# Performance work log

Hardware: AMD Instinct MI355X
Metric: run time of the kernel (lower is better)

## Reference

```python
import jax, jax.numpy as jnp
import numpy as np

# Llama-3-8B-like attention layer with ragged KV-cache attention (tp_size=1).
B = 4          # number of sequences in the ragged batch
NEW = 512      # new tokens per sequence
CACHE = 4096   # existing KV-cache length per sequence
TOTAL = CACHE + NEW
H = 32         # query heads
HKV = 8        # kv heads (GQA)
G = H // HKV   # query heads per kv head
D = 128        # head dim
HID = 4096     # hidden size
BSZ = B * NEW  # total ragged tokens
EPS = 1e-6
ROPE_THETA = 10000.0


def rotate_half(x):
    x1, x2 = jnp.split(x, 2, axis=-1)
    return jnp.concatenate([-x2, x1], axis=-1)


def setup_inputs() -> dict:
    key = jax.random.key(0)
    ks = jax.random.split(key, 8)
    hidden_states = jax.random.normal(ks[0], (BSZ, HID), jnp.float32)
    # per-token absolute positions: each sequence continues from CACHE
    pos = jnp.tile(CACHE + jnp.arange(NEW), B).astype(jnp.float32)  # [BSZ]
    inv_freq = 1.0 / (ROPE_THETA ** (jnp.arange(0, D, 2, dtype=jnp.float32) / D))
    ang = pos[:, None] * inv_freq[None, :]              # [BSZ, D/2]
    emb = jnp.concatenate([ang, ang], axis=-1)          # [BSZ, D]
    cos, sin = jnp.cos(emb), jnp.sin(emb)
    ln_weight = jnp.ones((HID,), jnp.float32)
    wq = jax.random.normal(ks[1], (HID, H * D), jnp.float32) * 0.02
    wk = jax.random.normal(ks[2], (HID, HKV * D), jnp.float32) * 0.02
    wv = jax.random.normal(ks[3], (HID, HKV * D), jnp.float32) * 0.02
    wo = jax.random.normal(ks[4], (H * D, HID), jnp.float32) * 0.02
    # pre-populated KV cache (first CACHE slots are live history; tail gets overwritten)
    k_cache = jax.random.normal(ks[5], (B, TOTAL, HKV, D), jnp.float32) * 0.5
    v_cache = jax.random.normal(ks[6], (B, TOTAL, HKV, D), jnp.float32) * 0.5
    return {"hidden_states": hidden_states, "cos": cos, "sin": sin,
            "ln_weight": ln_weight, "wq": wq, "wk": wk, "wv": wv, "wo": wo,
            "k_cache": k_cache, "v_cache": v_cache}


def reference(hidden_states, cos, sin, ln_weight, wq, wk, wv, wo, k_cache, v_cache):
    residual = hidden_states
    # RMSNorm (fp32 math, as in the torch module)
    x = hidden_states.astype(jnp.float32)
    var = jnp.mean(x * x, axis=-1, keepdims=True)
    hn = ln_weight * (x * jax.lax.rsqrt(var + EPS))
    # QKV projections (ragged: [tokens, heads, D])
    q = (hn @ wq).reshape(BSZ, H, D)
    k = (hn @ wk).reshape(BSZ, HKV, D)
    v = (hn @ wv).reshape(BSZ, HKV, D)
    # RoPE with unsqueeze_dim=1
    c, s = cos[:, None, :], sin[:, None, :]
    q = q * c + rotate_half(q) * s
    k = k * c + rotate_half(k) * s
    # un-ragged view: [B, NEW, heads, D]
    qb = q.reshape(B, NEW, H, D)
    kb = k.reshape(B, NEW, HKV, D)
    vb = v.reshape(B, NEW, HKV, D)
    # append new K/V into the cache
    kc = k_cache.at[:, CACHE:TOTAL].set(kb)
    vc = v_cache.at[:, CACHE:TOTAL].set(vb)
    # GQA attention against full cache, causal over absolute positions
    qg = qb.reshape(B, NEW, HKV, G, D)
    scores = jnp.einsum('bqhgd,bshd->bhgqs', qg, kc) * (1.0 / np.sqrt(D))
    qpos = CACHE + jnp.arange(NEW)
    mask = jnp.arange(TOTAL)[None, :] <= qpos[:, None]       # [NEW, TOTAL]
    scores = jnp.where(mask[None, None, None], scores, -1e30)
    p = jax.nn.softmax(scores, axis=-1)
    out = jnp.einsum('bhgqs,bshd->bqhgd', p, vc).reshape(BSZ, H * D)
    o = out @ wo
    return residual + o
```

## Files before the change

### kernel.cpp

```cpp
#include <hip/hip_runtime.h>
#include <hip/hip_bf16.h>

typedef __attribute__((ext_vector_type(8))) short short8;
typedef __attribute__((ext_vector_type(4))) float floatx4;
typedef __attribute__((ext_vector_type(16))) float f32x16;

#define B_C 4
#define NEW_C 512
#define CACHE_C 4096
#define TOTAL_C 4608
#define H_C 32
#define HKV_C 8
#define D_C 128
#define HID_C 4096
#define QKV_N 6144

__device__ __forceinline__ unsigned short f2bf(float f) {
  union { float f; unsigned u; } v; v.f = f;
  unsigned r = v.u + 0x7FFFu + ((v.u >> 16) & 1u);
  return (unsigned short)(r >> 16);
}
__device__ __forceinline__ float bf2f(unsigned short h) {
  union { unsigned u; float f; } v; v.u = ((unsigned)h) << 16; return v.f;
}
__device__ __forceinline__ unsigned pack_bf16(float lo, float hi) {
  return ((unsigned)f2bf(hi) << 16) | (unsigned)f2bf(lo);
}
__device__ __forceinline__ unsigned pack_trunc(float lo, float hi) {
  union { float f; unsigned u; } a, b;
  a.f = lo; b.f = hi;
  return __builtin_amdgcn_perm(b.u, a.u, 0x07060302u);
}
__device__ __forceinline__ void gload_lds16(const unsigned short* g, unsigned short* lds) {
  __builtin_amdgcn_global_load_lds(
      (const __attribute__((address_space(1))) unsigned int*)g,
      (__attribute__((address_space(3))) unsigned int*)lds, 16, 0, 0);
}

__global__ __launch_bounds__(256) void rmsnorm_k(const float* __restrict__ x,
                                                 const float* __restrict__ g,
                                                 unsigned short* __restrict__ hn) {
  const int row = blockIdx.x;
  const int t = threadIdx.x;
  const float4* xr = (const float4*)(x + (size_t)row * 4096);
  float4 v[4];
  float ss = 0.f;
#pragma unroll
  for (int i = 0; i < 4; ++i) {
    v[i] = xr[t + i * 256];
    ss += v[i].x * v[i].x + v[i].y * v[i].y + v[i].z * v[i].z + v[i].w * v[i].w;
  }
#pragma unroll
  for (int m = 1; m < 64; m <<= 1) ss += __shfl_xor(ss, m);
  __shared__ float red[4];
  if ((t & 63) == 0) red[t >> 6] = ss;
  __syncthreads();
  ss = red[0] + red[1] + red[2] + red[3];
  const float inv = rsqrtf(ss * (1.f / 4096.f) + 1e-6f);
  const float4* gw = (const float4*)g;
#pragma unroll
  for (int i = 0; i < 4; ++i) {
    float4 w4 = gw[t + i * 256];
    ushort4 o;
    o.x = f2bf(v[i].x * inv * w4.x);
    o.y = f2bf(v[i].y * inv * w4.y);
    o.z = f2bf(v[i].z * inv * w4.z);
    o.w = f2bf(v[i].w * inv * w4.w);
    *(ushort4*)&hn[(size_t)row * 4096 + (t + i * 256) * 4] = o;
  }
}

__global__ __launch_bounds__(256) void build_wqkvT_k(const float* __restrict__ wq,
                                                     const float* __restrict__ wk,
                                                     const float* __restrict__ wv,
                                                     unsigned short* __restrict__ out) {
  __shared__ float tile[32][33];
  const int n0 = blockIdx.x * 32, k0 = blockIdx.y * 32;
  const float* src; int ld, nc;
  if (n0 < 4096)      { src = wq; ld = 4096; nc = n0; }
  else if (n0 < 5120) { src = wk; ld = 1024; nc = n0 - 4096; }
  else                { src = wv; ld = 1024; nc = n0 - 5120; }
  const int t = threadIdx.x, r = t >> 3, cv = (t & 7) * 4;
  const float4 v = *(const float4*)&src[(size_t)(k0 + r) * ld + nc + cv];
  tile[r][cv + 0] = v.x; tile[r][cv + 1] = v.y; tile[r][cv + 2] = v.z; tile[r][cv + 3] = v.w;
  __syncthreads();
  ushort4 o;
  o.x = f2bf(tile[cv + 0][r]); o.y = f2bf(tile[cv + 1][r]);
  o.z = f2bf(tile[cv + 2][r]); o.w = f2bf(tile[cv + 3][r]);
  *(ushort4*)&out[(size_t)(n0 + r) * 4096 + k0 + cv] = o;
}

__global__ __launch_bounds__(256) void transpose_cvt_k(const float* __restrict__ src,
                                                       long sbs_hi, long sbs_lo, int sld,
                                                       unsigned short* __restrict__ dst,
                                                       long dbs, int dld) {
  __shared__ float tile[32][33];
  const int z = blockIdx.z;
  const long sb = (long)(z >> 3) * sbs_hi + (long)(z & 7) * sbs_lo;
  const long db = (long)z * dbs;
  const int r0 = blockIdx.y * 32, c0 = blockIdx.x * 32;
  const int t = threadIdx.x, r = t >> 3, cv = (t & 7) * 4;
  const float4 v = *(const float4*)&src[sb + (long)(r0 + r) * sld + c0 + cv];
  tile[r][cv + 0] = v.x; tile[r][cv + 1] = v.y; tile[r][cv + 2] = v.z; tile[r][cv + 3] = v.w;
  __syncthreads();
  ushort4 o;
  o.x = f2bf(tile[cv + 0][r]); o.y = f2bf(tile[cv + 1][r]);
  o.z = f2bf(tile[cv + 2][r]); o.w = f2bf(tile[cv + 3][r]);
  *(ushort4*)&dst[db + (long)(c0 + r) * dld + r0 + cv] = o;
}

__global__ __launch_bounds__(256) void transpose_u16_k(const unsigned short* __restrict__ src,
                                                       long sbs, int sld,
                                                       unsigned short* __restrict__ dst,
                                                       long dbs, int dld) {
  __shared__ unsigned short tile[32][36];
  const int z = blockIdx.z;
  const long sb = (long)z * sbs;
  const long db = (long)z * dbs;
  const int r0 = blockIdx.y * 32, c0 = blockIdx.x * 32;
  const int t = threadIdx.x, r = t >> 3, cv = (t & 7) * 4;
  const ushort4 v = *(const ushort4*)&src[sb + (long)(r0 + r) * sld + c0 + cv];
  tile[r][cv + 0] = v.x; tile[r][cv + 1] = v.y; tile[r][cv + 2] = v.z; tile[r][cv + 3] = v.w;
  __syncthreads();
  ushort4 o;
  o.x = tile[cv + 0][r]; o.y = tile[cv + 1][r]; o.z = tile[cv + 2][r]; o.w = tile[cv + 3][r];
  *(ushort4*)&dst[db + (long)(c0 + r) * dld + r0 + cv] = o;
}

__global__ __launch_bounds__(256) void cvt_kcache_k(const float* __restrict__ kc,
                                                    unsigned short* __restrict__ Kall) {
  const long i = (long)blockIdx.x * 256 + threadIdx.x;
  const long c = i & 31, s = (i >> 5) & 4095, h = (i >> 17) & 7, b = i >> 20;
  const float4 v = *(const float4*)&kc[((b * 4608 + s) * 8 + h) * 128 + c * 4];
  ushort4 o;
  o.x = f2bf(v.x); o.y = f2bf(v.y); o.z = f2bf(v.z); o.w = f2bf(v.w);
  *(ushort4*)&Kall[((b * 8 + h) * 4608L + s) * 128 + c * 4] = o;
}

__global__ __launch_bounds__(256) void rope_k(const unsigned short* __restrict__ qkv,
                                              const float* __restrict__ cosb,
                                              const float* __restrict__ sinb,
                                              unsigned short* __restrict__ qr,
                                              unsigned short* __restrict__ Kall) {
  const float SCL = 0.08838834764831845f * 1.4426950408889634f;
  const int row = blockIdx.x;
  const int b = row >> 9, n = row & 511;
  const unsigned short* src = qkv + (size_t)row * QKV_N;
  const float* cr = cosb + (size_t)row * 128;
  const float* sr = sinb + (size_t)row * 128;
  const int t = threadIdx.x;
#pragma unroll
  for (int i = 0; i < 8; ++i) {
    int pid = t + i * 256;
    int hd = pid >> 6, d = pid & 63;
    int idx = hd * 128 + d;
    float a = bf2f(src[idx]), bb = bf2f(src[idx + 64]);
    float c0 = cr[d], s0 = sr[d], c1 = cr[d + 64], s1 = sr[d + 64];
    qr[(size_t)row * 4096 + idx] = f2bf((a * c0 - bb * s0) * SCL);
    qr[(size_t)row * 4096 + idx + 64] = f2bf((bb * c1 + a * s1) * SCL);
  }
#pragma unroll
  for (int i = 0; i < 2; ++i) {
    int pid = t + i * 256;
    int hd = pid >> 6, d = pid & 63;
    float a = bf2f(src[4096 + hd * 128 + d]), bb = bf2f(src[4096 + hd * 128 + d + 64]);
    float c0 = cr[d], s0 = sr[d], c1 = cr[d + 64], s1 = sr[d + 64];
    long kb = ((long)(b * 8 + hd) * TOTAL_C + CACHE_C + n) * 128 + d;
    Kall[kb] = f2bf(a * c0 - bb * s0);
    Kall[kb + 64] = f2bf(bb * c1 + a * s1);
  }
}

template <int EPI>
__global__ __launch_bounds__(256) void gemm_bt(const unsigned short* __restrict__ A,
                                               const unsigned short* __restrict__ BT,
                                               unsigned short* __restrict__ Cbf,
                                               float* __restrict__ Cf,
                                               const float* __restrict__ resid,
                                               int M, int N, int K) {
  __shared__ unsigned short As[128 * 32];
  __shared__ unsigned short Bs[128 * 32];
  const int n0 = blockIdx.x * 128, m0 = blockIdx.y * 128;
  const int t = threadIdx.x, w = t >> 6, l = t & 63;
  const int l15 = l & 15, lhi = l >> 4;
  const int wm = (w >> 1) * 64, wn = (w & 1) * 64;
  floatx4 acc[4][4];
#pragma unroll
  for (int mt = 0; mt < 4; ++mt)
#pragma unroll
    for (int nt = 0; nt < 4; ++nt)
#pragma unroll
      for (int r = 0; r < 4; ++r) acc[mt][nt][r] = 0.f;

  const int c0 = w * 2, c1 = w * 2 + 1;
  const unsigned short* ga0 = A + (size_t)(m0 + c0 * 16 + (l >> 2)) * K + (l & 3) * 8;
  const unsigned short* ga1 = A + (size_t)(m0 + c1 * 16 + (l >> 2)) * K + (l & 3) * 8;
  const unsigned short* gb0 = BT + (size_t)(n0 + c0 * 16 + (l >> 2)) * K + (l & 3) * 8;
  const unsigned short* gb1 = BT + (size_t)(n0 + c1 * 16 + (l >> 2)) * K + (l & 3) * 8;
  unsigned short* lA0 = &As[c0 * 512];
  unsigned short* lA1 = &As[c1 * 512];
  unsigned short* lB0 = &Bs[c0 * 512];
  unsigned short* lB1 = &Bs[c1 * 512];

  for (int k0 = 0; k0 < K; k0 += 32) {
    gload_lds16(ga0 + k0, lA0);
    gload_lds16(ga1 + k0, lA1);
    gload_lds16(gb0 + k0, lB0);
    gload_lds16(gb1 + k0, lB1);
    __syncthreads();
    short8 af[4], bfv[4];
#pragma unroll
    for (int i = 0; i < 4; ++i) {
      af[i] = *(const short8*)&As[(wm + i * 16 + l15) * 32 + lhi * 8];
      bfv[i] = *(const short8*)&Bs[(wn + i * 16 + l15) * 32 + lhi * 8];
    }
#pragma unroll
    for (int mt = 0; mt < 4; ++mt)
#pragma unroll
      for (int nt = 0; nt < 4; ++nt)
        acc[mt][nt] = __builtin_amdgcn_mfma_f32_16x16x32_bf16(af[mt], bfv[nt], acc[mt][nt], 0, 0, 0);
    __syncthreads();
  }
#pragma unroll
  for (int mt = 0; mt < 4; ++mt)
#pragma unroll
    for (int nt = 0; nt < 4; ++nt)
#pragma unroll
      for (int r = 0; r < 4; ++r) {
        const int row = m0 + wm + mt * 16 + lhi * 4 + r;
        const int col = n0 + wn + nt * 16 + l15;
        const size_t idx = (size_t)row * N + col;
        if (EPI == 0) Cbf[idx] = f2bf(acc[mt][nt][r]);
        else Cf[idx] = acc[mt][nt][r] + resid[idx];
      }
}

__global__ __launch_bounds__(256, 2) void attn3_k(const unsigned short* __restrict__ Q,
                                                  const unsigned short* __restrict__ Kall,
                                                  const unsigned short* __restrict__ VT,
                                                  unsigned short* __restrict__ O) {
  __shared__ unsigned short Ks[2][8192];
  __shared__ unsigned short Vs[2][8192];
  __shared__ unsigned short ot[4][32][40];
  const int bid = blockIdx.x;
  const int swz = (bid & 7) * 64 + (bid >> 3);
  const int qt = swz & 15, hk = (swz >> 4) & 7, b = swz >> 7;
  const int t = threadIdx.x, w = t >> 6, l = t & 63;
  const int q5 = l & 31, h = l >> 5;
  const bool lo_half = (h == 0);

  const int nq = qt * 32 + w * 8 + (q5 >> 2);
  const int g = q5 & 3;
  const int qpos = CACHE_C + nq;

  const unsigned short* Kb = Kall + (size_t)(b * 8 + hk) * TOTAL_C * 128;
  const unsigned short* Vb = VT + (size_t)(b * 8 + hk) * 128 * TOTAL_C;

  const unsigned short* ksrc[4];
  const unsigned short* vsrc[4];
#pragma unroll
  for (int j = 0; j < 4; ++j) {
    const int c = w * 256 + j * 64 + l;
    const int sck = c ^ ((c >> 4) & 7);
    ksrc[j] = Kb + sck * 8;
    const int scv = c ^ ((c >> 3) & 7);
    vsrc[j] = Vb + (size_t)(c >> 3) * TOTAL_C + (scv & 7) * 8;
  }

  const int xmask = (q5 & 7) << 4;
  int kb_[8], vb_[4];
#pragma unroll
  for (int ks = 0; ks < 8; ++ks) kb_[ks] = q5 * 256 + ((ks * 32 + h * 16) ^ xmask);
#pragma unroll
  for (int f = 0; f < 4; ++f) vb_[f] = q5 * 128 + ((f * 32 + h * 16) ^ xmask);

  short8 qf[8];
  {
    const unsigned short* qrow =
        Q + (size_t)(b * 512 + nq) * 4096 + (hk * 4 + g) * 128 + h * 8;
#pragma unroll
    for (int ks = 0; ks < 8; ++ks) qf[ks] = *(const short8*)(qrow + ks * 16);
  }

  f32x16 oacc[4];
#pragma unroll
  for (int d = 0; d < 4; ++d)
#pragma unroll
    for (int r = 0; r < 16; ++r) oacc[d][r] = 0.f;
  float m = -1e30f, lsum = 0.f;

  const int nblk = ((CACHE_C + qt * 32 + 31) >> 6) + 1;

#pragma unroll
  for (int j = 0; j < 4; ++j) gload_lds16(ksrc[j], &Ks[0][w * 2048 + j * 512]);
#pragma unroll
  for (int j = 0; j < 4; ++j) gload_lds16(vsrc[j], &Vs[0][w * 2048 + j * 512]);

  for (int sb = 0; sb < nblk; ++sb) {
    __syncthreads();
    if (sb + 1 < nblk) {
      const int p1 = (sb + 1) & 1;
#pragma unroll
      for (int j = 0; j < 4; ++j)
        gload_lds16(ksrc[j] + (sb + 1) * 8192, &Ks[p1][w * 2048 + j * 512]);
#pragma unroll
      for (int j = 0; j < 4; ++j)
        gload_lds16(vsrc[j] + (sb + 1) * 64, &Vs[p1][w * 2048 + j * 512]);
      __builtin_amdgcn_sched_barrier(0);
    }
    const int s0 = sb << 6;
    const char* kp = (const char*)&Ks[sb & 1][0];
    const char* vp = (const char*)&Vs[sb & 1][0];

    f32x16 sa0, sa1;
#pragma unroll
    for (int r = 0; r < 16; ++r) { sa0[r] = 0.f; sa1[r] = 0.f; }
#pragma unroll
    for (int ks = 0; ks < 8; ++ks) {
      short8 k0 = *(const short8*)(kp + kb_[ks]);
      short8 k1 = *(const short8*)(kp + kb_[ks] + 8192);
      sa0 = __builtin_amdgcn_mfma_f32_32x32x16_bf16(k0, qf[ks], sa0, 0, 0, 0);
      sa1 = __builtin_amdgcn_mfma_f32_32x32x16_bf16(k1, qf[ks], sa1, 0, 0, 0);
    }
    if (sb == nblk - 1) {
#pragma unroll
      for (int r = 0; r < 16; ++r) {
        const int sg = s0 + ((r & 3) + 8 * (r >> 2) + 4 * h);
        if (sg > qpos) sa0[r] = -1e30f;
        if (sg + 32 > qpos) sa1[r] = -1e30f;
      }
    }
    float m8[8];
#pragma unroll
    for (int i = 0; i < 8; ++i)
      m8[i] = fmaxf(fmaxf(sa0[i], sa0[i + 8]), fmaxf(sa1[i], sa1[i + 8]));
#pragma unroll
    for (int st = 4; st >= 1; st >>= 1)
#pragma unroll
      for (int i = 0; i < st; ++i) m8[i] = fmaxf(m8[i], m8[i + st]);
    const float pmax = fmaxf(m8[0], __shfl_xor(m8[0], 32));
    if (__any(pmax > m)) {
      const float mn = fmaxf(m, pmax);
      const float sco = __builtin_amdgcn_exp2f(m - mn);
      m = mn;
      lsum *= sco;
#pragma unroll
      for (int d = 0; d < 4; ++d)
#pragma unroll
        for (int r = 0; r < 16; ++r) oacc[d][r] *= sco;
    }
    unsigned pk[16], sw[16];
    float s16[16];
#pragma unroll
    for (int i = 0; i < 8; ++i) {
      const float a0 = __builtin_amdgcn_exp2f(sa0[2 * i] - m);
      const float a1 = __builtin_amdgcn_exp2f(sa0[2 * i + 1] - m);
      const float b0 = __builtin_amdgcn_exp2f(sa1[2 * i] - m);
      const float b1 = __builtin_amdgcn_exp2f(sa1[2 * i + 1] - m);
      pk[i] = pack_trunc(a0, a1);
      pk[i + 8] = pack_trunc(b0, b1);
      s16[i] = a0 + a1;
      s16[i + 8] = b0 + b1;
    }
#pragma unroll
    for (int st = 8; st >= 1; st >>= 1)
#pragma unroll
      for (int i = 0; i < st; ++i) s16[i] += s16[i + st];
    lsum += s16[0];
#pragma unroll
    for (int i = 0; i < 16; ++i) sw[i] = __shfl_xor((int)pk[i], 32);
#pragma unroll
    for (int f = 0; f < 4; ++f) {
      union { int4 i4; short8 s8; } fr;
      fr.i4.x = lo_half ? pk[4 * f + 0] : sw[4 * f + 2];
      fr.i4.y = lo_half ? pk[4 * f + 1] : sw[4 * f + 3];
      fr.i4.z = lo_half ? sw[4 * f + 0] : pk[4 * f + 2];
      fr.i4.w = lo_half ? sw[4 * f + 1] : pk[4 * f + 3];
#pragma unroll
      for (int d = 0; d < 4; ++d) {
        short8 vf = *(const short8*)(vp + vb_[f] + d * 4096);
        oacc[d] = __builtin_amdgcn_mfma_f32_32x32x16_bf16(vf, fr.s8, oacc[d], 0, 0, 0);
      }
    }
  }

  lsum += __shfl_xor(lsum, 32);
  const float inv = 1.f / lsum;
#pragma unroll
  for (int db = 0; db < 4; ++db) {
    __syncthreads();
#pragma unroll
    for (int r = 0; r < 16; r += 2) {
      const float v0 = oacc[db][r] * inv;
      const float v1 = oacc[db][r + 1] * inv;
      const int dloc = (r & 3) + 8 * (r >> 2) + 4 * h;
      *(unsigned*)&ot[w][q5][dloc] = pack_bf16(v0, v1);
    }
    __syncthreads();
    const int qr_ = l >> 1, half = l & 1;
    const short8 ov0 = *(const short8*)&ot[w][qr_][half * 16];
    const short8 ov1 = *(const short8*)&ot[w][qr_][half * 16 + 8];
    const int n2 = qt * 32 + w * 8 + (qr_ >> 2), g2 = qr_ & 3;
    const size_t ob = (size_t)(b * 512 + n2) * 4096 + (hk * 4 + g2) * 128 + db * 32 + half * 16;
    *(short8*)&O[ob] = ov0;
    *(short8*)&O[ob + 8] = ov1;
  }
}

extern "C" void kernel_launch(void* const* d_in, const int* in_sizes, int n_in,
                              void* d_out, int out_size, void* d_ws, size_t ws_size,
                              hipStream_t stream) {
  const float* x = (const float*)d_in[0];
  const float* cosb = (const float*)d_in[1];
  const float* sinb = (const float*)d_in[2];
  const float* lnw = (const float*)d_in[3];
  const float* wq = (const float*)d_in[4];
  const float* wk = (const float*)d_in[5];
  const float* wv = (const float*)d_in[6];
  const float* wo = (const float*)d_in[7];
  const float* kcache = (const float*)d_in[8];
  const float* vcache = (const float*)d_in[9];
  float* out = (float*)d_out;
  char* ws = (char*)d_ws;

  unsigned short* hn    = (unsigned short*)(ws + 0);
  unsigned short* wqkvT = (unsigned short*)(ws + 16777216);
  unsigned short* qkv   = (unsigned short*)(ws + 67108864);
  unsigned short* qrope = (unsigned short*)(ws + 92274688);
  unsigned short* Kall  = (unsigned short*)(ws + 109051904);
  unsigned short* VallT = (unsigned short*)(ws + 146800640);
  unsigned short* attno = hn;
  unsigned short* woT   = wqkvT;

  rmsnorm_k<<<2048, 256, 0, stream>>>(x, lnw, hn);
  build_wqkvT_k<<<dim3(192, 128), 256, 0, stream>>>(wq, wk, wv, wqkvT);
  gemm_bt<0><<<dim3(48, 16), 256, 0, stream>>>(hn, wqkvT, qkv, nullptr, nullptr, 2048, 6144, 4096);
  rope_k<<<2048, 256, 0, stream>>>(qkv, cosb, sinb, qrope, Kall);
  transpose_u16_k<<<dim3(32, 16, 4), 256, 0, stream>>>(qkv + 5120, 512L * QKV_N, QKV_N,
                                                       VallT + CACHE_C, 4718592L, TOTAL_C);
  cvt_kcache_k<<<16384, 256, 0, stream>>>(kcache, Kall);
  transpose_cvt_k<<<dim3(4, 128, 32), 256, 0, stream>>>(vcache, 4718592L, 128L, 1024,
                                                        VallT, 589824L, TOTAL_C);
  attn3_k<<<512, 256, 0, stream>>>(qrope, Kall, VallT, attno);
  transpose_cvt_k<<<dim3(128, 128, 1), 256, 0, stream>>>(wo, 0L, 0L, 4096, woT, 0L, 4096);
  gemm_bt<1><<<dim3(32, 16), 256, 0, stream>>>(attno, woT, nullptr, out, x, 2048, 4096, 4096);
}
```

Baseline: 543.0 us.

## Replace GEMM with 8-wave double-buffered ping-pong kernel using 128x256 tiles

Replaces the simple single-buffered 128x128 bf16 GEMM with a 512-thread kernel on 128x256 tiles and BK=64. It double-buffers LDS with async global-to-LDS loads interleaved between four MFMA phases, and uses explicit vmcnt waits, barriers and setprio to overlap memory with compute. It also adds an XOR swizzle on LDS rows to avoid bank conflicts, and an XCD-aware block remap for L2 locality. The cost is much more LDS (96KB) and register pressure, plus hand-tuned wait counts that are fragile.

```diff
diff --git a/kernel.cpp b/kernel.cpp
--- a/kernel.cpp
+++ b/kernel.cpp
@@ -172,67 +172,197 @@
 }
 
 template <int EPI>
-__global__ __launch_bounds__(256) void gemm_bt(const unsigned short* __restrict__ A,
-                                               const unsigned short* __restrict__ BT,
-                                               unsigned short* __restrict__ Cbf,
-                                               float* __restrict__ Cf,
-                                               const float* __restrict__ resid,
-                                               int M, int N, int K) {
-  __shared__ unsigned short As[128 * 32];
-  __shared__ unsigned short Bs[128 * 32];
-  const int n0 = blockIdx.x * 128, m0 = blockIdx.y * 128;
+__global__ __launch_bounds__(512, 2) void gemm8p_k(const unsigned short* __restrict__ A,
+                                                   const unsigned short* __restrict__ BT,
+                                                   unsigned short* __restrict__ Cbf,
+                                                   float* __restrict__ Cf,
+                                                   const float* __restrict__ resid,
+                                                   int M, int N, int K, int nbx) {
+  __shared__ __align__(1024) unsigned short lds[49152];
   const int t = threadIdx.x, w = t >> 6, l = t & 63;
   const int l15 = l & 15, lhi = l >> 4;
-  const int wm = (w >> 1) * 64, wn = (w & 1) * 64;
+  const int wm = w >> 2, wn = w & 3;
+
+  const int nwg = gridDim.x, per = nwg >> 3;
+  const int bid = blockIdx.x;
+  const int swz = (bid & 7) * per + (bid >> 3);
+  const int by = swz / nbx, bx = swz % nbx;
+  const int m0 = by * 128, n0 = bx * 256;
+
+  const unsigned short *srcA0, *srcA1, *srcB00, *srcB01, *srcB10, *srcB11;
+  {
+    const int c = t >> 6, u = t & 63, r16 = u >> 2, jj = u & 3;
+    const int xr = (r16 >> 1) & 3;
+    const int row = (c >> 1) * 16 + r16;
+    const int kk = (c & 1) * 32 + (jj ^ xr) * 8;
+    const int c1 = 8 + c;
+    const int row1 = (c1 >> 1) * 16 + r16;
+    const int kk1 = (c1 & 1) * 32 + (jj ^ xr) * 8;
+    srcA0  = A + (size_t)(m0 + row) * K + kk;
+    srcA1  = A + (size_t)(m0 + 64 + row) * K + kk;
+    srcB00 = BT + (size_t)(n0 + row) * K + kk;
+    srcB01 = BT + (size_t)(n0 + row1) * K + kk1;
+    srcB10 = BT + (size_t)(n0 + 128 + row) * K + kk;
+    srcB11 = BT + (size_t)(n0 + 128 + row1) * K + kk1;
+  }
+  unsigned short* ldsA[2][2];
+  unsigned short* ldsB[2][2][2];
+#pragma unroll
+  for (int d = 0; d < 2; ++d) {
+#pragma unroll
+    for (int h = 0; h < 2; ++h) {
+      ldsA[d][h] = &lds[d * 8192 + h * 4096 + w * 512];
+#pragma unroll
+      for (int p = 0; p < 2; ++p)
+        ldsB[d][h][p] = &lds[16384 + d * 16384 + h * 8192 + p * 4096 + w * 512];
+    }
+  }
+  const int tail = l15 * 64 + ((lhi ^ ((l15 >> 1) & 3))) * 16;
+  int aro[2][2], bro[2][2];
+#pragma unroll
+  for (int mi = 0; mi < 2; ++mi)
+#pragma unroll
+    for (int ks = 0; ks < 2; ++ks) aro[mi][ks] = ((wm * 2 + mi) * 2 + ks) * 1024 + tail;
+#pragma unroll
+  for (int ni = 0; ni < 2; ++ni)
+#pragma unroll
+    for (int ks = 0; ks < 2; ++ks) bro[ni][ks] = ((wn * 2 + ni) * 2 + ks) * 1024 + tail;
+
   floatx4 acc[4][4];
 #pragma unroll
-  for (int mt = 0; mt < 4; ++mt)
-#pragma unroll
-    for (int nt = 0; nt < 4; ++nt)
-#pragma unroll
-      for (int r = 0; r < 4; ++r) acc[mt][nt][r] = 0.f;
-
-  const int c0 = w * 2, c1 = w * 2 + 1;
-  const unsigned short* ga0 = A + (size_t)(m0 + c0 * 16 + (l >> 2)) * K + (l & 3) * 8;
-  const unsigned short* ga1 = A + (size_t)(m0 + c1 * 16 + (l >> 2)) * K + (l & 3) * 8;
-  const unsigned short* gb0 = BT + (size_t)(n0 + c0 * 16 + (l >> 2)) * K + (l & 3) * 8;
-  const unsigned short* gb1 = BT + (size_t)(n0 + c1 * 16 + (l >> 2)) * K + (l & 3) * 8;
-  unsigned short* lA0 = &As[c0 * 512];
-  unsigned short* lA1 = &As[c1 * 512];
-  unsigned short* lB0 = &Bs[c0 * 512];
-  unsigned short* lB1 = &Bs[c1 * 512];
-
-  for (int k0 = 0; k0 < K; k0 += 32) {
-    gload_lds16(ga0 + k0, lA0);
-    gload_lds16(ga1 + k0, lA1);
-    gload_lds16(gb0 + k0, lB0);
-    gload_lds16(gb1 + k0, lB1);
-    __syncthreads();
-    short8 af[4], bfv[4];
-#pragma unroll
-    for (int i = 0; i < 4; ++i) {
-      af[i] = *(const short8*)&As[(wm + i * 16 + l15) * 32 + lhi * 8];
-      bfv[i] = *(const short8*)&Bs[(wn + i * 16 + l15) * 32 + lhi * 8];
-    }
-#pragma unroll
-    for (int mt = 0; mt < 4; ++mt)
-#pragma unroll
-      for (int nt = 0; nt < 4; ++nt)
-        acc[mt][nt] = __builtin_amdgcn_mfma_f32_16x16x32_bf16(af[mt], bfv[nt], acc[mt][nt], 0, 0, 0);
-    __syncthreads();
-  }
-#pragma unroll
-  for (int mt = 0; mt < 4; ++mt)
-#pragma unroll
-    for (int nt = 0; nt < 4; ++nt)
-#pragma unroll
-      for (int r = 0; r < 4; ++r) {
-        const int row = m0 + wm + mt * 16 + lhi * 4 + r;
-        const int col = n0 + wn + nt * 16 + l15;
-        const size_t idx = (size_t)row * N + col;
-        if (EPI == 0) Cbf[idx] = f2bf(acc[mt][nt][r]);
-        else Cf[idx] = acc[mt][nt][r] + resid[idx];
-      }
+  for (int i = 0; i < 4; ++i)
+#pragma unroll
+    for (int j = 0; j < 4; ++j)
+#pragma unroll
+      for (int r = 0; r < 4; ++r) acc[i][j][r] = 0.f;
+
+  gload_lds16(srcA0, ldsA[0][0]);
+  gload_lds16(srcB00, ldsB[0][0][0]);
+  gload_lds16(srcB01, ldsB[0][0][1]);
+  gload_lds16(srcA1, ldsA[0][1]);
+  gload_lds16(srcB10, ldsB[0][1][0]);
+  gload_lds16(srcB11, ldsB[0][1][1]);
+  asm volatile("s_waitcnt vmcnt(3)" ::: "memory");
+  __builtin_amdgcn_s_barrier();
+  __builtin_amdgcn_sched_barrier(0);
+
+  const int nt = K >> 6;
+  const char* ldsc = (const char*)lds;
+  for (int kt = 0; kt < nt; ++kt) {
+    const int d = kt & 1, dn = d ^ 1;
+    const bool pf = (kt + 1 < nt);
+    const int ko1 = (kt + 1) * 64;
+    const int aB0 = d * 16384;
+    const int aB1 = d * 16384 + 8192;
+    const int bB0 = 32768 + d * 32768;
+    const int bB1 = 32768 + d * 32768 + 16384;
+    short8 afA[2][2], afB[2][2], bf[2][2];
+
+#pragma unroll
+    for (int mi = 0; mi < 2; ++mi)
+#pragma unroll
+      for (int ks = 0; ks < 2; ++ks) afA[mi][ks] = *(const short8*)(ldsc + aB0 + aro[mi][ks]);
+#pragma unroll
+    for (int ni = 0; ni < 2; ++ni)
+#pragma unroll
+      for (int ks = 0; ks < 2; ++ks) bf[ni][ks] = *(const short8*)(ldsc + bB0 + bro[ni][ks]);
+    if (pf) {
+      gload_lds16(srcA0 + ko1, ldsA[dn][0]);
+      gload_lds16(srcB00 + ko1, ldsB[dn][0][0]);
+    }
+    __builtin_amdgcn_s_barrier();
+    __builtin_amdgcn_sched_barrier(0);
+    __builtin_amdgcn_s_setprio(1);
+#pragma unroll
+    for (int mi = 0; mi < 2; ++mi)
+#pragma unroll
+      for (int ni = 0; ni < 2; ++ni)
+#pragma unroll
+        for (int ks = 0; ks < 2; ++ks)
+          acc[mi][ni] = __builtin_amdgcn_mfma_f32_16x16x32_bf16(afA[mi][ks], bf[ni][ks], acc[mi][ni], 0, 0, 0);
+    __builtin_amdgcn_s_setprio(0);
+    if (pf) { asm volatile("s_waitcnt vmcnt(4)" ::: "memory"); }
+    else    { asm volatile("s_waitcnt vmcnt(2)" ::: "memory"); }
+    __builtin_amdgcn_s_barrier();
+    __builtin_amdgcn_sched_barrier(0);
+
+#pragma unroll
+    for (int mi = 0; mi < 2; ++mi)
+#pragma unroll
+      for (int ks = 0; ks < 2; ++ks) afB[mi][ks] = *(const short8*)(ldsc + aB1 + aro[mi][ks]);
+    if (pf) gload_lds16(srcB01 + ko1, ldsB[dn][0][1]);
+    __builtin_amdgcn_s_barrier();
+    __builtin_amdgcn_sched_barrier(0);
+    __builtin_amdgcn_s_setprio(1);
+#pragma unroll
+    for (int mi = 0; mi < 2; ++mi)
+#pragma unroll
+      for (int ni = 0; ni < 2; ++ni)
+#pragma unroll
+        for (int ks = 0; ks < 2; ++ks)
+          acc[2 + mi][ni] = __builtin_amdgcn_mfma_f32_16x16x32_bf16(afB[mi][ks], bf[ni][ks], acc[2 + mi][ni], 0, 0, 0);
+    __builtin_amdgcn_s_setprio(0);
+    if (pf) { asm volatile("s_waitcnt vmcnt(3)" ::: "memory"); }
+    else    { asm volatile("s_waitcnt vmcnt(0)" ::: "memory"); }
+    __builtin_amdgcn_s_barrier();
+    __builtin_amdgcn_sched_barrier(0);
+
+#pragma unroll
+    for (int ni = 0; ni < 2; ++ni)
+#pragma unroll
+      for (int ks = 0; ks < 2; ++ks) bf[ni][ks] = *(const short8*)(ldsc + bB1 + bro[ni][ks]);
+    if (pf) gload_lds16(srcA1 + ko1, ldsA[dn][1]);
+    __builtin_amdgcn_s_barrier();
+    __builtin_amdgcn_sched_barrier(0);
+    __builtin_amdgcn_s_setprio(1);
+#pragma unroll
+    for (int mi = 0; mi < 2; ++mi)
+#pragma unroll
+      for (int ni = 0; ni < 2; ++ni)
+#pragma unroll
+        for (int ks = 0; ks < 2; ++ks)
+          acc[mi][2 + ni] = __builtin_amdgcn_mfma_f32_16x16x32_bf16(afA[mi][ks], bf[ni][ks], acc[mi][2 + ni], 0, 0, 0);
+    __builtin_amdgcn_s_setprio(0);
+    __builtin_amdgcn_s_barrier();
+    __builtin_amdgcn_sched_barrier(0);
+
+    if (pf) {
+      gload_lds16(srcB10 + ko1, ldsB[dn][1][0]);
+      gload_lds16(srcB11 + ko1, ldsB[dn][1][1]);
+    }
+    __builtin_amdgcn_s_barrier();
+    __builtin_amdgcn_sched_barrier(0);
+    __builtin_amdgcn_s_setprio(1);
+#pragma unroll
+    for (int mi = 0; mi < 2; ++mi)
+#pragma unroll
+      for (int ni = 0; ni < 2; ++ni)
+#pragma unroll
+        for (int ks = 0; ks < 2; ++ks)
+          acc[2 + mi][2 + ni] = __builtin_amdgcn_mfma_f32_16x16x32_bf16(afB[mi][ks], bf[ni][ks], acc[2 + mi][2 + ni], 0, 0, 0);
+    __builtin_amdgcn_s_setprio(0);
+    asm volatile("s_waitcnt vmcnt(3)" ::: "memory");
+    __builtin_amdgcn_s_barrier();
+    __builtin_amdgcn_sched_barrier(0);
+  }
+
+#pragma unroll
+  for (int qm = 0; qm < 2; ++qm)
+#pragma unroll
+    for (int mi = 0; mi < 2; ++mi)
+#pragma unroll
+      for (int qn = 0; qn < 2; ++qn)
+#pragma unroll
+        for (int ni = 0; ni < 2; ++ni)
+#pragma unroll
+          for (int r = 0; r < 4; ++r) {
+            const int row = m0 + qm * 64 + wm * 32 + mi * 16 + lhi * 4 + r;
+            const int col = n0 + qn * 128 + wn * 32 + ni * 16 + l15;
+            const size_t idx = (size_t)row * N + col;
+            const float v = acc[qm * 2 + mi][qn * 2 + ni][r];
+            if (EPI == 0) Cbf[idx] = f2bf(v);
+            else Cf[idx] = v + resid[idx];
+          }
 }
 
 __global__ __launch_bounds__(256, 2) void attn3_k(const unsigned short* __restrict__ Q,
@@ -434,7 +564,7 @@
 
   rmsnorm_k<<<2048, 256, 0, stream>>>(x, lnw, hn);
   build_wqkvT_k<<<dim3(192, 128), 256, 0, stream>>>(wq, wk, wv, wqkvT);
-  gemm_bt<0><<<dim3(48, 16), 256, 0, stream>>>(hn, wqkvT, qkv, nullptr, nullptr, 2048, 6144, 4096);
+  gemm8p_k<0><<<384, 512, 0, stream>>>(hn, wqkvT, qkv, nullptr, nullptr, 2048, 6144, 4096, 24);
   rope_k<<<2048, 256, 0, stream>>>(qkv, cosb, sinb, qrope, Kall);
   transpose_u16_k<<<dim3(32, 16, 4), 256, 0, stream>>>(qkv + 5120, 512L * QKV_N, QKV_N,
                                                        VallT + CACHE_C, 4718592L, TOTAL_C);
@@ -443,5 +573,5 @@
                                                         VallT, 589824L, TOTAL_C);
   attn3_k<<<512, 256, 0, stream>>>(qrope, Kall, VallT, attno);
   transpose_cvt_k<<<dim3(128, 128, 1), 256, 0, stream>>>(wo, 0L, 0L, 4096, woT, 0L, 4096);
-  gemm_bt<1><<<dim3(32, 16), 256, 0, stream>>>(attno, woT, nullptr, out, x, 2048, 4096, 4096);
-}
+  gemm8p_k<1><<<256, 512, 0, stream>>>(attno, woT, nullptr, out, x, 2048, 4096, 4096, 16);
+}
```

New measurement: 554.1 us. +2.0%, slower.
